# Performance work log

Hardware: AMD Instinct MI355X
Metric: run time of the kernel (lower is better)

Reference implementation:

```python
import jax, jax.numpy as jnp
import numpy as np

FIELD_DIMS = [1000000, 100000, 1008, 1004, 102, 1000, 500, 50, 112, 107]
B = 16384
EMB = 32
DENSE = 16
MLP = [256, 128, 64]
BN_EPS = 1e-5
V_TOTAL = int(np.sum(FIELD_DIMS))
OFFSETS = jnp.asarray(np.concatenate([[0], np.cumsum(FIELD_DIMS)[:-1]]), dtype=jnp.int64)


def _xavier(key, fan_out, fan_in):
    lim = float(np.sqrt(6.0 / (fan_in + fan_out)))
    return jax.random.uniform(key, (fan_out, fan_in), jnp.float32, -lim, lim)


def setup_inputs() -> dict:
    key = jax.random.key(0)
    ks = jax.random.split(key, 16)
    # per-field in-range indices, stacked to [B, n_fields]
    sparse_cols = [jax.random.randint(jax.random.fold_in(ks[0], i), (B,), 0, d)
                   for i, d in enumerate(FIELD_DIMS)]
    sparse_inputs = jnp.stack(sparse_cols, axis=1).astype(jnp.int64)
    dense_inputs = jax.random.normal(ks[1], (B, DENSE), jnp.float32)
    # concatenated embedding / first-order bias tables (same math as per-field nn.Embedding)
    emb_table = 0.01 * jax.random.normal(ks[2], (V_TOTAL, EMB), jnp.float32)
    bias_table = 0.01 * jax.random.normal(ks[3], (V_TOTAL, 1), jnp.float32)
    fm_bias = jnp.zeros((1,), jnp.float32)
    dims = [len(FIELD_DIMS) * EMB + DENSE] + MLP
    params = {}
    for li in range(len(MLP)):
        params[f"W{li}"] = _xavier(ks[4 + li], dims[li + 1], dims[li])
        params[f"b{li}"] = jnp.zeros((dims[li + 1],), jnp.float32)
        params[f"g{li}"] = jnp.ones((dims[li + 1],), jnp.float32)
        params[f"be{li}"] = jnp.zeros((dims[li + 1],), jnp.float32)
    Wo = _xavier(ks[10], 1, MLP[-1])
    bo = jnp.zeros((1,), jnp.float32)
    return dict(sparse_inputs=sparse_inputs, dense_inputs=dense_inputs,
                emb_table=emb_table, bias_table=bias_table, fm_bias=fm_bias,
                Wo=Wo, bo=bo, **params)


def reference(sparse_inputs, dense_inputs, emb_table, bias_table, fm_bias,
              Wo, bo, W0, b0, g0, be0, W1, b1, g1, be1, W2, b2, g2, be2):
    idx = sparse_inputs + OFFSETS[None, :]           # [B, F] global rows
    field_embs = emb_table[idx]                      # [B, F, E] multi-table gather
    # FM first order: sum of per-field scalar biases
    fm_first = bias_table[idx][..., 0].sum(axis=1)   # [B]
    # FM second order: 0.5 * sum_d ((sum_f e)^2 - sum_f e^2)
    s = field_embs.sum(axis=1)                       # [B, E]
    sq = (field_embs * field_embs).sum(axis=1)       # [B, E]
    fm_second = 0.5 * (s * s - sq).sum(axis=-1)      # [B]
    fm_out = fm_bias[0] + fm_first + fm_second
    # deep component (BatchNorm in eval mode at init stats: mean=0, var=1; dropout=identity)
    x = jnp.concatenate([field_embs.reshape(field_embs.shape[0], -1), dense_inputs], axis=-1)
    inv = 1.0 / jnp.sqrt(1.0 + BN_EPS)
    for W, b, g, be in ((W0, b0, g0, be0), (W1, b1, g1, be1), (W2, b2, g2, be2)):
        h = x @ W.T + b
        h = h * (g * inv) + be
        x = jax.nn.relu(h)
    deep_out = (x @ Wo.T + bo)[:, 0]
    return jax.nn.sigmoid(fm_out + deep_out)
```

## Files before the change

kernel.cpp:

```cpp
#include <hip/hip_runtime.h>
#include <hip/hip_bf16.h>
#include <math.h>

#define BROWS 16384
#define NF    10
#define EMB   32
#define DENSE 16
#define K0S   352
#define K0    336
#define N0    256
#define N1    128
#define N2    64
#define BN_INV 0.99999500003749969f

__constant__ int c_offsets[NF] = {
    0, 1000000, 1100000, 1101008, 1102012,
    1102114, 1103114, 1103614, 1103664, 1103776
};

typedef short  bf16x8 __attribute__((ext_vector_type(8)));
typedef float  f32x4  __attribute__((ext_vector_type(4)));

static __device__ __forceinline__ unsigned short f2bf(float x) {
    union { float f; unsigned u; } c; c.f = x;
    unsigned r = (c.u + 0x7FFFu + ((c.u >> 16) & 1u)) >> 16;
    return (unsigned short)r;
}
static __device__ __forceinline__ float bf2f(unsigned short u) {
    union { unsigned u; float f; } c; c.u = ((unsigned)u) << 16; return c.f;
}

__global__ __launch_bounds__(256) void k_gather_fm(
    const int*   __restrict__ sparse,
    const float* __restrict__ dense,
    const float* __restrict__ emb,
    const float* __restrict__ bias_tab,
    const float* __restrict__ fm_bias,
    unsigned short* __restrict__ x0,
    float* __restrict__ fm)
{
    int gt  = blockIdx.x * 256 + threadIdx.x;
    int row = gt >> 3;
    int l   = gt & 7;
    if (row >= BROWS) return;

    const float4* emb4 = (const float4*)emb;
    unsigned short* xr = x0 + (size_t)row * K0S;

    float4 s4 = make_float4(0.f, 0.f, 0.f, 0.f);
    float sq = 0.f, first = 0.f;

#pragma unroll
    for (int f = 0; f < NF; ++f) {
        int idx = sparse[row * NF + f] + c_offsets[f];
        float4 v = emb4[(size_t)idx * 8 + l];
        s4.x += v.x; s4.y += v.y; s4.z += v.z; s4.w += v.w;
        sq += v.x * v.x + v.y * v.y + v.z * v.z + v.w * v.w;
        if (l == 0) first += bias_tab[idx];
        ushort4 o;
        o.x = f2bf(v.x); o.y = f2bf(v.y); o.z = f2bf(v.z); o.w = f2bf(v.w);
        *(ushort4*)(xr + f * EMB + 4 * l) = o;
    }

    float ss = s4.x * s4.x + s4.y * s4.y + s4.z * s4.z + s4.w * s4.w;
#pragma unroll
    for (int off = 1; off < 8; off <<= 1) {
        ss += __shfl_xor(ss, off, 8);
        sq += __shfl_xor(sq, off, 8);
    }

    if (l < 4) {
        float4 dv = ((const float4*)dense)[row * 4 + l];
        ushort4 o;
        o.x = f2bf(dv.x); o.y = f2bf(dv.y); o.z = f2bf(dv.z); o.w = f2bf(dv.w);
        *(ushort4*)(xr + NF * EMB + 4 * l) = o;
    } else {
        ushort4 z = make_ushort4(0, 0, 0, 0);
        *(ushort4*)(xr + K0 + 4 * (l - 4)) = z;
    }

    if (l == 0) fm[row] = fm_bias[0] + first + 0.5f * (ss - sq);
}

template <int NR, int KSRC, int KDST>
__global__ __launch_bounds__(256) void k_wconv(
    const float* __restrict__ src, unsigned short* __restrict__ dst)
{
    int i = blockIdx.x * 256 + threadIdx.x;
    if (i >= NR * KDST) return;
    int r = i / KDST, c = i - r * KDST;
    float v = (c < KSRC) ? src[r * KSRC + c] : 0.f;
    dst[i] = f2bf(v);
}

template <int NOUT, int KS>
__global__ __launch_bounds__(256) void k_mfma_bn_relu(
    const unsigned short* __restrict__ A,
    const unsigned short* __restrict__ W,
    const float* __restrict__ b,
    const float* __restrict__ g,
    const float* __restrict__ be,
    unsigned short* __restrict__ C)
{
    const int tid  = threadIdx.x;
    const int wave = tid >> 6;
    const int lane = tid & 63;
    const int l16  = lane & 15;
    const int quad = lane >> 4;
    const int bm   = blockIdx.x * 128;
    const int bn   = blockIdx.y * 64;

    f32x4 acc[2][4];
#pragma unroll
    for (int i = 0; i < 2; ++i)
#pragma unroll
        for (int j = 0; j < 4; ++j) acc[i][j] = (f32x4){0.f, 0.f, 0.f, 0.f};

    const unsigned short* ap0 = A + (size_t)(bm + wave * 32 + l16) * KS + quad * 8;
    const unsigned short* ap1 = ap0 + (size_t)16 * KS;
    const unsigned short* wp0 = W + (size_t)(bn + l16) * KS + quad * 8;

#pragma unroll 1
    for (int k0 = 0; k0 < KS; k0 += 32) {
        bf16x8 a0 = *(const bf16x8*)(ap0 + k0);
        bf16x8 a1 = *(const bf16x8*)(ap1 + k0);
#pragma unroll
        for (int nt = 0; nt < 4; ++nt) {
            bf16x8 bw = *(const bf16x8*)(wp0 + (size_t)(16 * nt) * KS + k0);
            acc[0][nt] = __builtin_amdgcn_mfma_f32_16x16x32_bf16(a0, bw, acc[0][nt], 0, 0, 0);
            acc[1][nt] = __builtin_amdgcn_mfma_f32_16x16x32_bf16(a1, bw, acc[1][nt], 0, 0, 0);
        }
    }

#pragma unroll
    for (int nt = 0; nt < 4; ++nt) {
        int col = bn + 16 * nt + l16;
        float sc = g[col] * BN_INV;
        float tb = fmaf(b[col], sc, be[col]);
#pragma unroll
        for (int mt = 0; mt < 2; ++mt) {
#pragma unroll
            for (int r = 0; r < 4; ++r) {
                int row = bm + wave * 32 + 16 * mt + quad * 4 + r;
                float v = fmaf(acc[mt][nt][r], sc, tb);
                v = v > 0.f ? v : 0.f;
                C[(size_t)row * NOUT + col] = f2bf(v);
            }
        }
    }
}

__global__ __launch_bounds__(256) void k_final(
    const unsigned short* __restrict__ x3,
    const float* __restrict__ Wo,
    const float* __restrict__ bo,
    const float* __restrict__ fm,
    float* __restrict__ out)
{
    int row = blockIdx.x * 256 + threadIdx.x;
    if (row >= BROWS) return;
    const uint4* xq = (const uint4*)(x3 + (size_t)row * 64);
    float dot = 0.f;
#pragma unroll
    for (int q = 0; q < 8; ++q) {
        uint4 v = xq[q];
        const float* w = Wo + 8 * q;
        dot += bf2f(v.x & 0xFFFFu) * w[0] + bf2f(v.x >> 16) * w[1];
        dot += bf2f(v.y & 0xFFFFu) * w[2] + bf2f(v.y >> 16) * w[3];
        dot += bf2f(v.z & 0xFFFFu) * w[4] + bf2f(v.z >> 16) * w[5];
        dot += bf2f(v.w & 0xFFFFu) * w[6] + bf2f(v.w >> 16) * w[7];
    }
    float z = fm[row] + dot + bo[0];
    out[row] = 1.f / (1.f + expf(-z));
}

extern "C" void kernel_launch(void* const* d_in, const int* in_sizes, int n_in,
                              void* d_out, int out_size, void* d_ws, size_t ws_size,
                              hipStream_t stream)
{
    const int*   sparse   = (const int*)  d_in[0];
    const float* dense    = (const float*)d_in[1];
    const float* emb      = (const float*)d_in[2];
    const float* bias_tab = (const float*)d_in[3];
    const float* fm_bias  = (const float*)d_in[4];
    const float* Wo       = (const float*)d_in[5];
    const float* bo       = (const float*)d_in[6];
    const float* W0 = (const float*)d_in[7];
    const float* b0 = (const float*)d_in[8];
    const float* g0 = (const float*)d_in[9];
    const float* be0= (const float*)d_in[10];
    const float* W1 = (const float*)d_in[11];
    const float* b1 = (const float*)d_in[12];
    const float* g1 = (const float*)d_in[13];
    const float* be1= (const float*)d_in[14];
    const float* W2 = (const float*)d_in[15];
    const float* b2 = (const float*)d_in[16];
    const float* g2 = (const float*)d_in[17];
    const float* be2= (const float*)d_in[18];

    float* out = (float*)d_out;

    char* p = (char*)d_ws;
    unsigned short* x0  = (unsigned short*)p; p += (size_t)BROWS * K0S * 2;
    unsigned short* x1  = (unsigned short*)p; p += (size_t)BROWS * N0 * 2;
    unsigned short* x2  = (unsigned short*)p; p += (size_t)BROWS * N1 * 2;
    unsigned short* x3  = (unsigned short*)p; p += (size_t)BROWS * N2 * 2;
    unsigned short* W0b = (unsigned short*)p; p += (size_t)N0 * K0S * 2;
    unsigned short* W1b = (unsigned short*)p; p += (size_t)N1 * N0 * 2;
    unsigned short* W2b = (unsigned short*)p; p += (size_t)N2 * N1 * 2;
    float*          fm  = (float*)p;

    k_wconv<N0, K0, K0S><<<(N0 * K0S + 255) / 256, 256, 0, stream>>>(W0, W0b);
    k_wconv<N1, N0, N0 ><<<(N1 * N0  + 255) / 256, 256, 0, stream>>>(W1, W1b);
    k_wconv<N2, N1, N1 ><<<(N2 * N1  + 255) / 256, 256, 0, stream>>>(W2, W2b);

    k_gather_fm<<<(BROWS * 8) / 256, 256, 0, stream>>>(
        sparse, dense, emb, bias_tab, fm_bias, x0, fm);

    dim3 g0d(BROWS / 128, N0 / 64);
    k_mfma_bn_relu<N0, K0S><<<g0d, 256, 0, stream>>>(x0, W0b, b0, g0, be0, x1);
    dim3 g1d(BROWS / 128, N1 / 64);
    k_mfma_bn_relu<N1, N0 ><<<g1d, 256, 0, stream>>>(x1, W1b, b1, g1, be1, x2);
    dim3 g2d(BROWS / 128, N2 / 64);
    k_mfma_bn_relu<N2, N1 ><<<g2d, 256, 0, stream>>>(x2, W2b, b2, g2, be2, x3);

    k_final<<<BROWS / 256, 256, 0, stream>>>(x3, Wo, bo, fm, out);
}
```

Baseline: 244.5 us.

## Fuse embedding gather into layer-0 MFMA and fuse layers 1-2 with output head

Gathers embedding rows directly into the MFMA A-operand registers of the first layer, so the bf16 x0 activation buffer is never written or read back. Layers 1 and 2 and the final dot plus sigmoid now run in one kernel, with the layer-1 output staged in LDS. The three weight-conversion kernels become one launch. Together this cuts global traffic and kernel launches from eight to three. The cost is that each wave now holds sixteen 16x16 accumulators covering all 256 output columns, which raises register pressure and lowers occupancy.

```diff
diff --git a/kernel.cpp b/kernel.cpp
--- a/kernel.cpp
+++ b/kernel.cpp
@@ -26,152 +26,227 @@
     unsigned r = (c.u + 0x7FFFu + ((c.u >> 16) & 1u)) >> 16;
     return (unsigned short)r;
 }
-static __device__ __forceinline__ float bf2f(unsigned short u) {
-    union { unsigned u; float f; } c; c.u = ((unsigned)u) << 16; return c.f;
-}
-
-__global__ __launch_bounds__(256) void k_gather_fm(
+
+__global__ __launch_bounds__(256) void k_wconv_all(
+    const float* __restrict__ W0, const float* __restrict__ W1,
+    const float* __restrict__ W2,
+    unsigned short* __restrict__ W0b, unsigned short* __restrict__ W1b,
+    unsigned short* __restrict__ W2b)
+{
+    int i = blockIdx.x * 256 + threadIdx.x;
+    if (i < N0 * K0S) {
+        int r = i / K0S, c = i - r * K0S;
+        W0b[i] = f2bf(c < K0 ? W0[r * K0 + c] : 0.f);
+    } else if (i < N0 * K0S + N1 * N0) {
+        int j = i - N0 * K0S;
+        W1b[j] = f2bf(W1[j]);
+    } else {
+        int j = i - (N0 * K0S + N1 * N0);
+        W2b[j] = f2bf(W2[j]);
+    }
+}
+
+__global__ __launch_bounds__(256) void k_fused_l0(
     const int*   __restrict__ sparse,
     const float* __restrict__ dense,
     const float* __restrict__ emb,
     const float* __restrict__ bias_tab,
     const float* __restrict__ fm_bias,
-    unsigned short* __restrict__ x0,
+    const unsigned short* __restrict__ W0b,
+    const float* __restrict__ b0, const float* __restrict__ g0,
+    const float* __restrict__ be0,
+    unsigned short* __restrict__ x1,
     float* __restrict__ fm)
-{
-    int gt  = blockIdx.x * 256 + threadIdx.x;
-    int row = gt >> 3;
-    int l   = gt & 7;
-    if (row >= BROWS) return;
-
-    const float4* emb4 = (const float4*)emb;
-    unsigned short* xr = x0 + (size_t)row * K0S;
-
-    float4 s4 = make_float4(0.f, 0.f, 0.f, 0.f);
-    float sq = 0.f, first = 0.f;
-
-#pragma unroll
-    for (int f = 0; f < NF; ++f) {
-        int idx = sparse[row * NF + f] + c_offsets[f];
-        float4 v = emb4[(size_t)idx * 8 + l];
-        s4.x += v.x; s4.y += v.y; s4.z += v.z; s4.w += v.w;
-        sq += v.x * v.x + v.y * v.y + v.z * v.z + v.w * v.w;
-        if (l == 0) first += bias_tab[idx];
-        ushort4 o;
-        o.x = f2bf(v.x); o.y = f2bf(v.y); o.z = f2bf(v.z); o.w = f2bf(v.w);
-        *(ushort4*)(xr + f * EMB + 4 * l) = o;
-    }
-
-    float ss = s4.x * s4.x + s4.y * s4.y + s4.z * s4.z + s4.w * s4.w;
-#pragma unroll
-    for (int off = 1; off < 8; off <<= 1) {
-        ss += __shfl_xor(ss, off, 8);
-        sq += __shfl_xor(sq, off, 8);
-    }
-
-    if (l < 4) {
-        float4 dv = ((const float4*)dense)[row * 4 + l];
-        ushort4 o;
-        o.x = f2bf(dv.x); o.y = f2bf(dv.y); o.z = f2bf(dv.z); o.w = f2bf(dv.w);
-        *(ushort4*)(xr + NF * EMB + 4 * l) = o;
-    } else {
-        ushort4 z = make_ushort4(0, 0, 0, 0);
-        *(ushort4*)(xr + K0 + 4 * (l - 4)) = z;
-    }
-
-    if (l == 0) fm[row] = fm_bias[0] + first + 0.5f * (ss - sq);
-}
-
-template <int NR, int KSRC, int KDST>
-__global__ __launch_bounds__(256) void k_wconv(
-    const float* __restrict__ src, unsigned short* __restrict__ dst)
-{
-    int i = blockIdx.x * 256 + threadIdx.x;
-    if (i >= NR * KDST) return;
-    int r = i / KDST, c = i - r * KDST;
-    float v = (c < KSRC) ? src[r * KSRC + c] : 0.f;
-    dst[i] = f2bf(v);
-}
-
-template <int NOUT, int KS>
-__global__ __launch_bounds__(256) void k_mfma_bn_relu(
-    const unsigned short* __restrict__ A,
-    const unsigned short* __restrict__ W,
-    const float* __restrict__ b,
-    const float* __restrict__ g,
-    const float* __restrict__ be,
-    unsigned short* __restrict__ C)
 {
     const int tid  = threadIdx.x;
     const int wave = tid >> 6;
     const int lane = tid & 63;
     const int l16  = lane & 15;
     const int quad = lane >> 4;
-    const int bm   = blockIdx.x * 128;
-    const int bn   = blockIdx.y * 64;
-
-    f32x4 acc[2][4];
-#pragma unroll
-    for (int i = 0; i < 2; ++i)
-#pragma unroll
-        for (int j = 0; j < 4; ++j) acc[i][j] = (f32x4){0.f, 0.f, 0.f, 0.f};
-
-    const unsigned short* ap0 = A + (size_t)(bm + wave * 32 + l16) * KS + quad * 8;
-    const unsigned short* ap1 = ap0 + (size_t)16 * KS;
-    const unsigned short* wp0 = W + (size_t)(bn + l16) * KS + quad * 8;
-
-#pragma unroll 1
-    for (int k0 = 0; k0 < KS; k0 += 32) {
-        bf16x8 a0 = *(const bf16x8*)(ap0 + k0);
-        bf16x8 a1 = *(const bf16x8*)(ap1 + k0);
-#pragma unroll
-        for (int nt = 0; nt < 4; ++nt) {
-            bf16x8 bw = *(const bf16x8*)(wp0 + (size_t)(16 * nt) * KS + k0);
-            acc[0][nt] = __builtin_amdgcn_mfma_f32_16x16x32_bf16(a0, bw, acc[0][nt], 0, 0, 0);
-            acc[1][nt] = __builtin_amdgcn_mfma_f32_16x16x32_bf16(a1, bw, acc[1][nt], 0, 0, 0);
-        }
-    }
-
-#pragma unroll
-    for (int nt = 0; nt < 4; ++nt) {
-        int col = bn + 16 * nt + l16;
-        float sc = g[col] * BN_INV;
-        float tb = fmaf(b[col], sc, be[col]);
-#pragma unroll
-        for (int mt = 0; mt < 2; ++mt) {
-#pragma unroll
-            for (int r = 0; r < 4; ++r) {
-                int row = bm + wave * 32 + 16 * mt + quad * 4 + r;
-                float v = fmaf(acc[mt][nt][r], sc, tb);
-                v = v > 0.f ? v : 0.f;
-                C[(size_t)row * NOUT + col] = f2bf(v);
-            }
-        }
-    }
-}
-
-__global__ __launch_bounds__(256) void k_final(
-    const unsigned short* __restrict__ x3,
+    const int arow = blockIdx.x * 64 + wave * 16 + l16;
+
+    int idx[NF];
+#pragma unroll
+    for (int f = 0; f < NF; ++f)
+        idx[f] = sparse[arow * NF + f] + c_offsets[f];
+
+    float first = 0.f;
+    if (quad == 0) {
+#pragma unroll
+        for (int f = 0; f < NF; ++f) first += bias_tab[idx[f]];
+    }
+
+    float s8[8];
+#pragma unroll
+    for (int j = 0; j < 8; ++j) s8[j] = 0.f;
+    float sq = 0.f;
+
+    f32x4 acc[16];
+#pragma unroll
+    for (int nt = 0; nt < 16; ++nt) acc[nt] = (f32x4){0.f, 0.f, 0.f, 0.f};
+
+#pragma unroll
+    for (int f = 0; f < NF; ++f) {
+        const float4* ep = (const float4*)(emb + (size_t)idx[f] * EMB + quad * 8);
+        float4 v0 = ep[0];
+        float4 v1 = ep[1];
+        s8[0] += v0.x; s8[1] += v0.y; s8[2] += v0.z; s8[3] += v0.w;
+        s8[4] += v1.x; s8[5] += v1.y; s8[6] += v1.z; s8[7] += v1.w;
+        sq += v0.x*v0.x + v0.y*v0.y + v0.z*v0.z + v0.w*v0.w
+            + v1.x*v1.x + v1.y*v1.y + v1.z*v1.z + v1.w*v1.w;
+        bf16x8 a;
+        a[0] = (short)f2bf(v0.x); a[1] = (short)f2bf(v0.y);
+        a[2] = (short)f2bf(v0.z); a[3] = (short)f2bf(v0.w);
+        a[4] = (short)f2bf(v1.x); a[5] = (short)f2bf(v1.y);
+        a[6] = (short)f2bf(v1.z); a[7] = (short)f2bf(v1.w);
+        const unsigned short* wp = W0b + (size_t)l16 * K0S + f * 32 + quad * 8;
+#pragma unroll
+        for (int nt = 0; nt < 16; ++nt) {
+            bf16x8 w = *(const bf16x8*)(wp + (size_t)(nt * 16) * K0S);
+            acc[nt] = __builtin_amdgcn_mfma_f32_16x16x32_bf16(a, w, acc[nt], 0, 0, 0);
+        }
+    }
+
+    {
+        bf16x8 a;
+        if (quad < 2) {
+            const float4* dp = (const float4*)(dense + arow * DENSE + quad * 8);
+            float4 v0 = dp[0];
+            float4 v1 = dp[1];
+            a[0] = (short)f2bf(v0.x); a[1] = (short)f2bf(v0.y);
+            a[2] = (short)f2bf(v0.z); a[3] = (short)f2bf(v0.w);
+            a[4] = (short)f2bf(v1.x); a[5] = (short)f2bf(v1.y);
+            a[6] = (short)f2bf(v1.z); a[7] = (short)f2bf(v1.w);
+        } else {
+#pragma unroll
+            for (int j = 0; j < 8; ++j) a[j] = 0;
+        }
+        const unsigned short* wp = W0b + (size_t)l16 * K0S + 320 + quad * 8;
+#pragma unroll
+        for (int nt = 0; nt < 16; ++nt) {
+            bf16x8 w = *(const bf16x8*)(wp + (size_t)(nt * 16) * K0S);
+            acc[nt] = __builtin_amdgcn_mfma_f32_16x16x32_bf16(a, w, acc[nt], 0, 0, 0);
+        }
+    }
+
+    float ss = 0.f;
+#pragma unroll
+    for (int j = 0; j < 8; ++j) ss += s8[j] * s8[j];
+    ss += __shfl_xor(ss, 16); ss += __shfl_xor(ss, 32);
+    sq += __shfl_xor(sq, 16); sq += __shfl_xor(sq, 32);
+    first += __shfl_xor(first, 16); first += __shfl_xor(first, 32);
+    if (quad == 0)
+        fm[arow] = fm_bias[0] + first + 0.5f * (ss - sq);
+
+#pragma unroll
+    for (int nt = 0; nt < 16; ++nt) {
+        int col = nt * 16 + l16;
+        float sc = g0[col] * BN_INV;
+        float tb = fmaf(b0[col], sc, be0[col]);
+#pragma unroll
+        for (int r = 0; r < 4; ++r) {
+            int orow = blockIdx.x * 64 + wave * 16 + quad * 4 + r;
+            float v = fmaf(acc[nt][r], sc, tb);
+            v = v > 0.f ? v : 0.f;
+            x1[(size_t)orow * N0 + col] = f2bf(v);
+        }
+    }
+}
+
+__global__ __launch_bounds__(256) void k_fused_tail(
+    const unsigned short* __restrict__ x1,
+    const unsigned short* __restrict__ W1b,
+    const float* __restrict__ b1, const float* __restrict__ g1,
+    const float* __restrict__ be1,
+    const unsigned short* __restrict__ W2b,
+    const float* __restrict__ b2, const float* __restrict__ g2,
+    const float* __restrict__ be2,
     const float* __restrict__ Wo,
     const float* __restrict__ bo,
     const float* __restrict__ fm,
     float* __restrict__ out)
 {
-    int row = blockIdx.x * 256 + threadIdx.x;
-    if (row >= BROWS) return;
-    const uint4* xq = (const uint4*)(x3 + (size_t)row * 64);
-    float dot = 0.f;
-#pragma unroll
-    for (int q = 0; q < 8; ++q) {
-        uint4 v = xq[q];
-        const float* w = Wo + 8 * q;
-        dot += bf2f(v.x & 0xFFFFu) * w[0] + bf2f(v.x >> 16) * w[1];
-        dot += bf2f(v.y & 0xFFFFu) * w[2] + bf2f(v.y >> 16) * w[3];
-        dot += bf2f(v.z & 0xFFFFu) * w[4] + bf2f(v.z >> 16) * w[5];
-        dot += bf2f(v.w & 0xFFFFu) * w[6] + bf2f(v.w >> 16) * w[7];
-    }
-    float z = fm[row] + dot + bo[0];
-    out[row] = 1.f / (1.f + expf(-z));
+    __shared__ unsigned short h2[64][N1 + 8];
+
+    const int tid  = threadIdx.x;
+    const int wave = tid >> 6;
+    const int lane = tid & 63;
+    const int l16  = lane & 15;
+    const int quad = lane >> 4;
+    const int bm   = blockIdx.x * 64;
+    const int arow = bm + wave * 16 + l16;
+
+    f32x4 acc1[8];
+#pragma unroll
+    for (int nt = 0; nt < 8; ++nt) acc1[nt] = (f32x4){0.f, 0.f, 0.f, 0.f};
+    const unsigned short* ap1 = x1 + (size_t)arow * N0 + quad * 8;
+#pragma unroll
+    for (int ks = 0; ks < 8; ++ks) {
+        bf16x8 a = *(const bf16x8*)(ap1 + ks * 32);
+        const unsigned short* wp = W1b + (size_t)l16 * N0 + ks * 32 + quad * 8;
+#pragma unroll
+        for (int nt = 0; nt < 8; ++nt) {
+            bf16x8 w = *(const bf16x8*)(wp + (size_t)(nt * 16) * N0);
+            acc1[nt] = __builtin_amdgcn_mfma_f32_16x16x32_bf16(a, w, acc1[nt], 0, 0, 0);
+        }
+    }
+#pragma unroll
+    for (int nt = 0; nt < 8; ++nt) {
+        int col = nt * 16 + l16;
+        float sc = g1[col] * BN_INV;
+        float tb = fmaf(b1[col], sc, be1[col]);
+#pragma unroll
+        for (int r = 0; r < 4; ++r) {
+            float v = fmaf(acc1[nt][r], sc, tb);
+            v = v > 0.f ? v : 0.f;
+            h2[wave * 16 + quad * 4 + r][col] = f2bf(v);
+        }
+    }
+    __syncthreads();
+
+    f32x4 acc2[4];
+#pragma unroll
+    for (int nt = 0; nt < 4; ++nt) acc2[nt] = (f32x4){0.f, 0.f, 0.f, 0.f};
+#pragma unroll
+    for (int ks = 0; ks < 4; ++ks) {
+        bf16x8 a = *(const bf16x8*)(&h2[wave * 16 + l16][ks * 32 + quad * 8]);
+        const unsigned short* wp = W2b + (size_t)l16 * N1 + ks * 32 + quad * 8;
+#pragma unroll
+        for (int nt = 0; nt < 4; ++nt) {
+            bf16x8 w = *(const bf16x8*)(wp + (size_t)(nt * 16) * N1);
+            acc2[nt] = __builtin_amdgcn_mfma_f32_16x16x32_bf16(a, w, acc2[nt], 0, 0, 0);
+        }
+    }
+
+    float p[4] = {0.f, 0.f, 0.f, 0.f};
+#pragma unroll
+    for (int nt = 0; nt < 4; ++nt) {
+        int col = nt * 16 + l16;
+        float sc = g2[col] * BN_INV;
+        float tb = fmaf(b2[col], sc, be2[col]);
+        float wo = Wo[col];
+#pragma unroll
+        for (int r = 0; r < 4; ++r) {
+            float v = fmaf(acc2[nt][r], sc, tb);
+            v = v > 0.f ? v : 0.f;
+            p[r] = fmaf(v, wo, p[r]);
+        }
+    }
+#pragma unroll
+    for (int r = 0; r < 4; ++r) {
+        p[r] += __shfl_xor(p[r], 1);
+        p[r] += __shfl_xor(p[r], 2);
+        p[r] += __shfl_xor(p[r], 4);
+        p[r] += __shfl_xor(p[r], 8);
+    }
+    if (l16 == 0) {
+#pragma unroll
+        for (int r = 0; r < 4; ++r) {
+            int orow = bm + wave * 16 + quad * 4 + r;
+            float z = fm[orow] + p[r] + bo[0];
+            out[orow] = 1.f / (1.f + expf(-z));
+        }
+    }
 }
 
 extern "C" void kernel_launch(void* const* d_in, const int* in_sizes, int n_in,
@@ -201,28 +276,18 @@
     float* out = (float*)d_out;
 
     char* p = (char*)d_ws;
-    unsigned short* x0  = (unsigned short*)p; p += (size_t)BROWS * K0S * 2;
     unsigned short* x1  = (unsigned short*)p; p += (size_t)BROWS * N0 * 2;
-    unsigned short* x2  = (unsigned short*)p; p += (size_t)BROWS * N1 * 2;
-    unsigned short* x3  = (unsigned short*)p; p += (size_t)BROWS * N2 * 2;
     unsigned short* W0b = (unsigned short*)p; p += (size_t)N0 * K0S * 2;
     unsigned short* W1b = (unsigned short*)p; p += (size_t)N1 * N0 * 2;
     unsigned short* W2b = (unsigned short*)p; p += (size_t)N2 * N1 * 2;
     float*          fm  = (float*)p;
 
-    k_wconv<N0, K0, K0S><<<(N0 * K0S + 255) / 256, 256, 0, stream>>>(W0, W0b);
-    k_wconv<N1, N0, N0 ><<<(N1 * N0  + 255) / 256, 256, 0, stream>>>(W1, W1b);
-    k_wconv<N2, N1, N1 ><<<(N2 * N1  + 255) / 256, 256, 0, stream>>>(W2, W2b);
-
-    k_gather_fm<<<(BROWS * 8) / 256, 256, 0, stream>>>(
-        sparse, dense, emb, bias_tab, fm_bias, x0, fm);
-
-    dim3 g0d(BROWS / 128, N0 / 64);
-    k_mfma_bn_relu<N0, K0S><<<g0d, 256, 0, stream>>>(x0, W0b, b0, g0, be0, x1);
-    dim3 g1d(BROWS / 128, N1 / 64);
-    k_mfma_bn_relu<N1, N0 ><<<g1d, 256, 0, stream>>>(x1, W1b, b1, g1, be1, x2);
-    dim3 g2d(BROWS / 128, N2 / 64);
-    k_mfma_bn_relu<N2, N1 ><<<g2d, 256, 0, stream>>>(x2, W2b, b2, g2, be2, x3);
-
-    k_final<<<BROWS / 256, 256, 0, stream>>>(x3, Wo, bo, fm, out);
-}
+    k_wconv_all<<<(N0 * K0S + N1 * N0 + N2 * N1) / 256, 256, 0, stream>>>(
+        W0, W1, W2, W0b, W1b, W2b);
+
+    k_fused_l0<<<BROWS / 64, 256, 0, stream>>>(
+        sparse, dense, emb, bias_tab, fm_bias, W0b, b0, g0, be0, x1, fm);
+
+    k_fused_tail<<<BROWS / 64, 256, 0, stream>>>(
+        x1, W1b, b1, g1, be1, W2b, b2, g2, be2, Wo, bo, fm, out);
+}
```

After: 245.9 us. No clear change (+0.6%).
